# Kernel optimization log

Hardware: AMD Instinct MI355X
Metric: run time of the kernel (lower is better)

Reference implementation:

```python
import jax, jax.numpy as jnp
import numpy as np

BATCH, SEQ, E, H = 8, 2048, 1024, 1024
LEAK = 0.95
SPECTRAL_RADIUS = 1.2
SPARSITY = 0.1


def setup_inputs() -> dict:
    rng = np.random.default_rng(0)
    x = rng.standard_normal((BATCH, SEQ, E)).astype(np.float32)
    # W_in: kaiming_uniform-like init
    bound = np.sqrt(1.0 / E)
    W_in = rng.uniform(-bound, bound, (H, E)).astype(np.float32)
    # W_res: sparse normal, rescaled to spectral radius 1.2
    W_res = rng.standard_normal((H, H)).astype(np.float32)
    mask = (rng.random((H, H)) > SPARSITY).astype(np.float32)
    W_res *= mask
    rad = np.max(np.abs(np.linalg.eigvals(W_res.astype(np.float64))))
    W_res = (W_res * (SPECTRAL_RADIUS / (rad + 1e-8))).astype(np.float32)
    s = 0.02
    inp = {
        "x": jnp.asarray(x),
        "W_in": jnp.asarray(W_in),
        "W_res": jnp.asarray(W_res),
        "norm_g": jnp.ones((E,), jnp.float32),
        "norm_b": jnp.zeros((E,), jnp.float32),
        "delta_w": jnp.asarray(rng.standard_normal((1, E)).astype(np.float32) * s),
        "delta_b": jnp.zeros((1,), jnp.float32),
        "A": jnp.full((H,), -10.0, jnp.float32),
        "B_w": jnp.asarray(rng.standard_normal((H, E)).astype(np.float32) * s),
        "ro_g": jnp.ones((H,), jnp.float32),
        "ro_b": jnp.zeros((H,), jnp.float32),
        "ro_w": jnp.asarray(rng.standard_normal((E, H)).astype(np.float32) * s),
        "ro_bias": jnp.zeros((E,), jnp.float32),
        "gate_w": jnp.asarray(rng.standard_normal((E, E)).astype(np.float32) * s),
        "gate_b": jnp.zeros((E,), jnp.float32),
    }
    return inp


def _layernorm(x, g, b, eps=1e-5):
    m = jnp.mean(x, axis=-1, keepdims=True)
    v = jnp.mean((x - m) ** 2, axis=-1, keepdims=True)
    return (x - m) * jax.lax.rsqrt(v + eps) * g + b


def reference(x, W_in, W_res, norm_g, norm_b, delta_w, delta_b, A, B_w,
              ro_g, ro_b, ro_w, ro_bias, gate_w, gate_b):
    x_norm = _layernorm(x, norm_g, norm_b)                      # [B,S,E]

    # --- TrueReservoir: leaky tanh RNN (scan over seq) ---
    xin = jnp.einsum('bse,he->bsh', x_norm, W_in)               # [B,S,H]
    h0 = jnp.zeros((x.shape[0], W_res.shape[0]), x.dtype)

    def res_step(h, u):
        new = jnp.tanh(u + h @ W_res.T)
        new = LEAK * new + (1.0 - LEAK) * h
        return new, new

    _, res_states = jax.lax.scan(res_step, h0, jnp.swapaxes(xin, 0, 1))
    res_states = jnp.swapaxes(res_states, 0, 1)                 # [B,S,H]

    ro_in = _layernorm(res_states, ro_g, ro_b)
    reservoir_out = jax.nn.gelu(jnp.einsum('bsh,eh->bse', ro_in, ro_w) + ro_bias,
                                approximate=False)              # [B,S,E]

    # --- selective SSM-style scan ---
    Bx = jnp.einsum('bse,he->bsh', x_norm, B_w)                 # [B,S,H]
    delta = jax.nn.softplus(jnp.einsum('bse,oe->bso', x_norm, delta_w) + delta_b)  # [B,S,1]
    A_bar = jnp.exp(A * delta)                                  # [B,S,H]
    B_bar = Bx * (1.0 - A_bar) / (A + 1e-8)                     # [B,S,H]

    def ssm_step(h, ab):
        a, b = ab
        h = a * h + b
        return h, h

    _, ssm_states = jax.lax.scan(
        ssm_step, h0, (jnp.swapaxes(A_bar, 0, 1), jnp.swapaxes(B_bar, 0, 1)))
    ssm_states = jnp.swapaxes(ssm_states, 0, 1)                 # [B,S,H]

    gate = jax.nn.sigmoid(jnp.einsum('bse,fe->bsf', x, gate_w) + gate_b)  # [B,S,E]
    return reservoir_out * gate + ssm_states * (1.0 - gate)
```

## Files before the change

### kernel.cpp

```cpp
#include <hip/hip_runtime.h>
#include <math.h>

#define B_ 8
#define S_ 2048
#define E_ 1024
#define H_ 1024
#define M_ 16384

typedef __attribute__((ext_vector_type(8))) short short8;
typedef __attribute__((ext_vector_type(4))) float floatx4;

__device__ __forceinline__ void block_reduce2(float &a, float &b) {
#pragma unroll
  for (int off = 32; off > 0; off >>= 1) {
    a += __shfl_down(a, off);
    b += __shfl_down(b, off);
  }
  __shared__ float sa[4], sb[4];
  const int w = threadIdx.x >> 6;
  __syncthreads();
  if ((threadIdx.x & 63) == 0) { sa[w] = a; sb[w] = b; }
  __syncthreads();
  a = sa[0] + sa[1] + sa[2] + sa[3];
  b = sb[0] + sb[1] + sb[2] + sb[3];
}

__device__ __forceinline__ unsigned pack_bf16(float lo, float hi) {
  return __builtin_amdgcn_perm(__float_as_uint(hi) + 0x8000u,
                               __float_as_uint(lo) + 0x8000u, 0x07060302u);
}
__device__ __forceinline__ unsigned pack_hi16(unsigned a, unsigned b) {
  return __builtin_amdgcn_perm(b, a, 0x07060302u);
}

__global__ __launch_bounds__(256) void ln_delta_kernel(
    const float* __restrict__ x, const float* __restrict__ g, const float* __restrict__ bt,
    const float* __restrict__ dw, const float* __restrict__ db,
    unsigned short* __restrict__ xnb, float* __restrict__ delta)
{
  const int row = blockIdx.x;
  const int t = threadIdx.x;
  const float4 v = ((const float4*)(x + (size_t)row * E_))[t];
  float s1 = v.x + v.y + v.z + v.w;
  float s2 = v.x*v.x + v.y*v.y + v.z*v.z + v.w*v.w;
  block_reduce2(s1, s2);
  const float mean = s1 * (1.f / E_);
  const float var  = s2 * (1.f / E_) - mean * mean;
  const float rstd = rsqrtf(var + 1e-5f);
  const float4 g4 = ((const float4*)g)[t];
  const float4 b4 = ((const float4*)bt)[t];
  float4 o;
  o.x = (v.x - mean) * rstd * g4.x + b4.x;
  o.y = (v.y - mean) * rstd * g4.y + b4.y;
  o.z = (v.z - mean) * rstd * g4.z + b4.z;
  o.w = (v.w - mean) * rstd * g4.w + b4.w;
  uint2 p;
  p.x = pack_bf16(o.x, o.y); p.y = pack_bf16(o.z, o.w);
  ((uint2*)(xnb + (size_t)row * E_))[t] = p;
  const float4 d4 = ((const float4*)dw)[t];
  float dd = o.x*d4.x + o.y*d4.y + o.z*d4.z + o.w*d4.w;
  float dummy = 0.f;
  block_reduce2(dd, dummy);
  if (t == 0) {
    const float z = dd + db[0];
    delta[row] = (z > 20.f) ? z : log1pf(__expf(z));
  }
}

__global__ __launch_bounds__(256) void rowstats_kernel(
    const float* __restrict__ res, float2* __restrict__ st)
{
  const int row = blockIdx.x;
  const int t = threadIdx.x;
  const float4 v = ((const float4*)(res + (size_t)row * H_))[t];
  float s1 = v.x + v.y + v.z + v.w;
  float s2 = v.x*v.x + v.y*v.y + v.z*v.z + v.w*v.w;
  block_reduce2(s1, s2);
  if (t == 0) {
    const float m = s1 * (1.f / H_);
    const float var = s2 * (1.f / H_) - m * m;
    st[row] = make_float2(m, rsqrtf(var + 1e-5f));
  }
}

__global__ __launch_bounds__(256) void tobf16_kernel(
    const float* __restrict__ s, unsigned short* __restrict__ d)
{
  const int i = blockIdx.x * 256 + threadIdx.x;
  const float4 v = ((const float4*)s)[i];
  uint2 p;
  p.x = pack_bf16(v.x, v.y); p.y = pack_bf16(v.z, v.w);
  ((uint2*)d)[i] = p;
}

__global__ __launch_bounds__(256) void splitw_kernel(
    const float* __restrict__ s, unsigned short* __restrict__ dh, unsigned short* __restrict__ dl)
{
  const int i = blockIdx.x * 256 + threadIdx.x;
  const float4 v = ((const float4*)s)[i];
  const float sv[4] = {v.x, v.y, v.z, v.w};
  unsigned h[4]; float l[4];
#pragma unroll
  for (int e = 0; e < 4; ++e) {
    h[e] = (__float_as_uint(sv[e]) + 0x8000u) & 0xFFFF0000u;
    l[e] = sv[e] - __uint_as_float(h[e]);
  }
  uint2 ph, pl;
  ph.x = pack_hi16(h[0], h[1]); ph.y = pack_hi16(h[2], h[3]);
  pl.x = pack_bf16(l[0], l[1]); pl.y = pack_bf16(l[2], l[3]);
  ((uint2*)dh)[i] = ph;
  ((uint2*)dl)[i] = pl;
}

__global__ __launch_bounds__(256) void gemm_bb(
    const unsigned short* __restrict__ A, const unsigned short* __restrict__ W,
    float* __restrict__ C)
{
  __shared__ __align__(16) unsigned short As[128 * 40];
  __shared__ __align__(16) unsigned short Ws[128 * 40];
  const int tid  = threadIdx.x;
  const int bn   = blockIdx.x & 7;
  const int bm   = blockIdx.x >> 3;
  const int wave = tid >> 6, lane = tid & 63;
  const int wm = (wave >> 1) * 64, wn = (wave & 1) * 64;
  const int fm = lane & 15, quad = lane >> 4;

  floatx4 acc[4][4];
#pragma unroll
  for (int i = 0; i < 4; ++i)
#pragma unroll
    for (int j = 0; j < 4; ++j) acc[i][j] = (floatx4){0.f, 0.f, 0.f, 0.f};

  const unsigned short* Abase = A + (size_t)bm * 128 * 1024;
  const unsigned short* Wbase = W + (size_t)bn * 128 * 1024;

  for (int k0 = 0; k0 < 1024; k0 += 32) {
    uint2 a2[4], w2[4];
#pragma unroll
    for (int i = 0; i < 4; ++i) {
      const int q = tid + 256 * i;
      const int row = q >> 3, ch = q & 7;
      a2[i] = *(const uint2*)(Abase + (size_t)row * 1024 + k0 + ch * 4);
      w2[i] = *(const uint2*)(Wbase + (size_t)row * 1024 + k0 + ch * 4);
    }
#pragma unroll
    for (int i = 0; i < 4; ++i) {
      const int q = tid + 256 * i;
      const int row = q >> 3, ch = q & 7;
      *(uint2*)(&As[row * 40 + ch * 4]) = a2[i];
      *(uint2*)(&Ws[row * 40 + ch * 4]) = w2[i];
    }
    __syncthreads();
    short8 af[4], wf[4];
#pragma unroll
    for (int i = 0; i < 4; ++i) {
      af[i] = *(const short8*)(&As[(wm + i * 16 + fm) * 40 + quad * 8]);
      wf[i] = *(const short8*)(&Ws[(wn + i * 16 + fm) * 40 + quad * 8]);
    }
#pragma unroll
    for (int i = 0; i < 4; ++i)
#pragma unroll
      for (int j = 0; j < 4; ++j)
        acc[i][j] = __builtin_amdgcn_mfma_f32_16x16x32_bf16(af[i], wf[j], acc[i][j], 0, 0, 0);
    __syncthreads();
  }

#pragma unroll
  for (int i = 0; i < 4; ++i) {
    const int grow0 = bm * 128 + wm + i * 16 + quad * 4;
#pragma unroll
    for (int j = 0; j < 4; ++j) {
      const int gcol = bn * 128 + wn + j * 16 + fm;
#pragma unroll
      for (int r = 0; r < 4; ++r)
        C[(size_t)(grow0 + r) * 1024 + gcol] = acc[i][j][r];
    }
  }
}

template<int ACT>
__global__ __launch_bounds__(256) void gemm_bf16_nt(
    const float* __restrict__ A, const float* __restrict__ W,
    const float* __restrict__ bias, float* __restrict__ C)
{
  __shared__ __align__(16) unsigned short As[128 * 40];
  __shared__ __align__(16) unsigned short Ws[128 * 40];
  const int tid  = threadIdx.x;
  const int bn   = blockIdx.x & 7;
  const int bm   = blockIdx.x >> 3;
  const int wave = tid >> 6, lane = tid & 63;
  const int wm = (wave >> 1) * 64, wn = (wave & 1) * 64;
  const int fm = lane & 15, quad = lane >> 4;

  floatx4 acc[4][4];
#pragma unroll
  for (int i = 0; i < 4; ++i)
#pragma unroll
    for (int j = 0; j < 4; ++j) acc[i][j] = (floatx4){0.f, 0.f, 0.f, 0.f};

  const float* Abase = A + (size_t)bm * 128 * 1024;
  const float* Wbase = W + (size_t)bn * 128 * 1024;

  for (int k0 = 0; k0 < 1024; k0 += 32) {
    float4 a4[4], w4[4];
#pragma unroll
    for (int i = 0; i < 4; ++i) {
      const int q = tid + 256 * i;
      const int row = q >> 3, ch = q & 7;
      a4[i] = *(const float4*)(Abase + (size_t)row * 1024 + k0 + ch * 4);
      w4[i] = *(const float4*)(Wbase + (size_t)row * 1024 + k0 + ch * 4);
    }
#pragma unroll
    for (int i = 0; i < 4; ++i) {
      const int q = tid + 256 * i;
      const int row = q >> 3, ch = q & 7;
      uint2 pa, pw;
      pa.x = pack_bf16(a4[i].x, a4[i].y); pa.y = pack_bf16(a4[i].z, a4[i].w);
      pw.x = pack_bf16(w4[i].x, w4[i].y); pw.y = pack_bf16(w4[i].z, w4[i].w);
      *(uint2*)(&As[row * 40 + ch * 4]) = pa;
      *(uint2*)(&Ws[row * 40 + ch * 4]) = pw;
    }
    __syncthreads();
    short8 af[4], wf[4];
#pragma unroll
    for (int i = 0; i < 4; ++i) {
      af[i] = *(const short8*)(&As[(wm + i * 16 + fm) * 40 + quad * 8]);
      wf[i] = *(const short8*)(&Ws[(wn + i * 16 + fm) * 40 + quad * 8]);
    }
#pragma unroll
    for (int i = 0; i < 4; ++i)
#pragma unroll
      for (int j = 0; j < 4; ++j)
        acc[i][j] = __builtin_amdgcn_mfma_f32_16x16x32_bf16(af[i], wf[j], acc[i][j], 0, 0, 0);
    __syncthreads();
  }

#pragma unroll
  for (int i = 0; i < 4; ++i) {
    const int grow0 = bm * 128 + wm + i * 16 + quad * 4;
#pragma unroll
    for (int j = 0; j < 4; ++j) {
      const int gcol = bn * 128 + wn + j * 16 + fm;
      const float bb = (ACT == 1) ? bias[gcol] : 0.f;
#pragma unroll
      for (int r = 0; r < 4; ++r) {
        float v = acc[i][j][r] + bb;
        if (ACT == 1) v = 1.f / (1.f + __expf(-v));
        C[(size_t)(grow0 + r) * 1024 + gcol] = v;
      }
    }
  }
}

__global__ __launch_bounds__(256) void gemm_readout_mfma(
    const float* __restrict__ A,
    const unsigned short* __restrict__ Wh_g,
    const unsigned short* __restrict__ Wl_g,
    const float* __restrict__ bias,
    const float2* __restrict__ lnst,
    const float* __restrict__ lng, const float* __restrict__ lnb,
    const float* __restrict__ Avec,
    const float* __restrict__ cumd,
    const float* __restrict__ chH,
    const float* __restrict__ gate,
    float* __restrict__ C)
{
  __shared__ __align__(16) unsigned short Ah[128 * 40];
  __shared__ __align__(16) unsigned short Al[128 * 40];
  __shared__ __align__(16) unsigned short Wh[128 * 40];
  __shared__ __align__(16) unsigned short Wl[128 * 40];
  const int tid  = threadIdx.x;
  const int bn   = blockIdx.x & 7;
  const int bm   = blockIdx.x >> 3;
  const int wave = tid >> 6, lane = tid & 63;
  const int wm = (wave >> 1) * 64, wn = (wave & 1) * 64;
  const int fm = lane & 15, quad = lane >> 4;

  floatx4 acc[4][4];
#pragma unroll
  for (int i = 0; i < 4; ++i)
#pragma unroll
    for (int j = 0; j < 4; ++j) acc[i][j] = (floatx4){0.f, 0.f, 0.f, 0.f};

  const float* Abase = A + (size_t)bm * 128 * 1024;
  const unsigned short* Whb = Wh_g + (size_t)bn * 128 * 1024;
  const unsigned short* Wlb = Wl_g + (size_t)bn * 128 * 1024;

  float2 st_i[4];
#pragma unroll
  for (int i = 0; i < 4; ++i) {
    const int q = tid + 256 * i;
    st_i[i] = lnst[bm * 128 + (q >> 3)];
  }

  for (int k0 = 0; k0 < 1024; k0 += 32) {
#pragma unroll
    for (int i = 0; i < 4; ++i) {
      const int q = tid + 256 * i;
      const int row = q >> 3, ch = q & 7;
      float4 a4 = *(const float4*)(Abase + (size_t)row * 1024 + k0 + ch * 4);
      const float4 g4 = *(const float4*)(lng + k0 + ch * 4);
      const float4 b4 = *(const float4*)(lnb + k0 + ch * 4);
      const float2 st = st_i[i];
      a4.x = (a4.x - st.x) * st.y * g4.x + b4.x;
      a4.y = (a4.y - st.x) * st.y * g4.y + b4.y;
      a4.z = (a4.z - st.x) * st.y * g4.z + b4.z;
      a4.w = (a4.w - st.x) * st.y * g4.w + b4.w;
      const float av[4] = {a4.x, a4.y, a4.z, a4.w};
      unsigned ah[4]; float alr[4];
#pragma unroll
      for (int e = 0; e < 4; ++e) {
        ah[e] = (__float_as_uint(av[e]) + 0x8000u) & 0xFFFF0000u;
        alr[e] = av[e] - __uint_as_float(ah[e]);
      }
      uint2 pah, pal;
      pah.x = pack_hi16(ah[0], ah[1]); pah.y = pack_hi16(ah[2], ah[3]);
      pal.x = pack_bf16(alr[0], alr[1]); pal.y = pack_bf16(alr[2], alr[3]);
      *(uint2*)(&Ah[row * 40 + ch * 4]) = pah;
      *(uint2*)(&Al[row * 40 + ch * 4]) = pal;
      *(uint2*)(&Wh[row * 40 + ch * 4]) = *(const uint2*)(Whb + (size_t)row * 1024 + k0 + ch * 4);
      *(uint2*)(&Wl[row * 40 + ch * 4]) = *(const uint2*)(Wlb + (size_t)row * 1024 + k0 + ch * 4);
    }
    __syncthreads();
    short8 afh[4], afl[4], wfh[4], wfl[4];
#pragma unroll
    for (int i = 0; i < 4; ++i) {
      const int ao = (wm + i * 16 + fm) * 40 + quad * 8;
      const int wo = (wn + i * 16 + fm) * 40 + quad * 8;
      afh[i] = *(const short8*)(&Ah[ao]);
      afl[i] = *(const short8*)(&Al[ao]);
      wfh[i] = *(const short8*)(&Wh[wo]);
      wfl[i] = *(const short8*)(&Wl[wo]);
    }
#pragma unroll
    for (int i = 0; i < 4; ++i)
#pragma unroll
      for (int j = 0; j < 4; ++j) {
        acc[i][j] = __builtin_amdgcn_mfma_f32_16x16x32_bf16(afh[i], wfh[j], acc[i][j], 0, 0, 0);
        acc[i][j] = __builtin_amdgcn_mfma_f32_16x16x32_bf16(afl[i], wfh[j], acc[i][j], 0, 0, 0);
        acc[i][j] = __builtin_amdgcn_mfma_f32_16x16x32_bf16(afh[i], wfl[j], acc[i][j], 0, 0, 0);
      }
    __syncthreads();
  }

#pragma unroll
  for (int i = 0; i < 4; ++i) {
    const int grow0 = bm * 128 + wm + i * 16 + quad * 4;
    float cd_r[4];
    int hb_r[4];
#pragma unroll
    for (int r = 0; r < 4; ++r) {
      const int gr = grow0 + r;
      const int b = gr >> 11;
      const int c = (gr & 2047) >> 7;
      cd_r[r] = cumd[gr];
      hb_r[r] = (b * 16 + c) << 10;
    }
#pragma unroll
    for (int j = 0; j < 4; ++j) {
      const int gcol = bn * 128 + wn + j * 16 + fm;
      const float Ae = Avec[gcol];
      const float bb = bias[gcol];
#pragma unroll
      for (int r = 0; r < 4; ++r) {
        const int gr = grow0 + r;
        const size_t off = (size_t)gr * 1024 + gcol;
        const float hin = chH[hb_r[r] + gcol];
        const float lcl = C[off];
        const float gt  = gate[off];
        float v = acc[i][j][r] + bb;
        v = 0.5f * v * (1.f + erff(v * 0.70710678118654752f));
        const float p = __expf(Ae * cd_r[r]);
        const float sst = lcl + p * hin;
        C[off] = v * gt + sst * (1.f - gt);
      }
    }
  }
}

__global__ __launch_bounds__(512, 2) void reservoir_scan_kernel(
    float* __restrict__ xin_res,
    const float* __restrict__ Wres,
    unsigned* __restrict__ hbuf,
    unsigned* __restrict__ unused)
{
  const int tid = threadIdx.x;
  const int wg  = blockIdx.x;
  const int go  = wg >> 4;
  const int mem = wg & 15;
  const int g   = tid >> 6;
  const int l   = tid & 63;
  const int c   = l & 7;
  const int rl  = l >> 3;
  const int row = mem * 64 + g * 8 + rl;

  __shared__ __align__(16) float hs[2][1024];

  float4 w4r[32];
  {
    const float* wrow = Wres + (size_t)row * 1024 + c * 128;
#pragma unroll
    for (int i = 0; i < 32; ++i)
      w4r[i] = *(const float4*)(wrow + 4 * ((i + c) & 31));
  }

  float hprev = 0.f;
  const unsigned long long tmask = 0x0000FFFF0000FFFFull;

  for (int s = 0; s < S_; ++s) {
    const float u = xin_res[((size_t)go * S_ + s) * H_ + row];
    asm volatile("" :: "v"(u));

    const unsigned tag = (unsigned)s & 0xFFFFu;
    const unsigned long long tag2 = (unsigned long long)tag | ((unsigned long long)tag << 32);
    const unsigned long long* hp =
        (const unsigned long long*)(hbuf + (size_t)(s & 1) * 8192 + go * 1024) + tid;
    unsigned long long w;
    for (;;) {
      w = __hip_atomic_load(hp, __ATOMIC_RELAXED, __HIP_MEMORY_SCOPE_AGENT);
      if (((w ^ tag2) & tmask) == 0ull) break;
    }

    float2 hf;
    hf.x = __uint_as_float((unsigned)w & 0xFFFF0000u);
    hf.y = __uint_as_float((unsigned)(w >> 32) & 0xFFFF0000u);
    *(float2*)(&hs[s & 1][2 * tid]) = hf;
    __syncthreads();

    const float* hc = &hs[s & 1][c * 128];
    float p0 = 0.f, p1 = 0.f, p2 = 0.f, p3 = 0.f;
#pragma unroll
    for (int i = 0; i < 32; ++i) {
      const float4 h4 = *(const float4*)(hc + 4 * ((i + c) & 31));
      p0 += w4r[i].x * h4.x;
      p1 += w4r[i].y * h4.y;
      p2 += w4r[i].z * h4.z;
      p3 += w4r[i].w * h4.w;
    }
    float ps = (p0 + p1) + (p2 + p3);
    ps += __shfl_xor(ps, 1);
    ps += __shfl_xor(ps, 2);
    ps += __shfl_xor(ps, 4);

    const float z  = u + ps;
    const float e  = __expf(2.f * z);
    const float hn = 1.f - __fdividef(2.f, e + 1.f);
    const float hv = 0.95f * hn + 0.05f * hprev;
    hprev = hv;

    if (c == 0) {
      const unsigned word = ((__float_as_uint(hv) + 0x8000u) & 0xFFFF0000u)
                          | ((unsigned)(s + 1) & 0xFFFFu);
      __hip_atomic_store(hbuf + (size_t)((s + 1) & 1) * 8192 + go * 1024 + row, word,
                         __ATOMIC_RELAXED, __HIP_MEMORY_SCOPE_AGENT);
      xin_res[((size_t)go * S_ + s) * H_ + row] = hv;
    }
  }
}

__global__ __launch_bounds__(128) void cumd_kernel(
    const float* __restrict__ delta, float* __restrict__ cumd)
{
  const int t = threadIdx.x;
  const int b = t >> 4, c = t & 15;
  const int base = b * S_ + c * 128;
  float acc = 0.f;
  for (int i = 0; i < 128; ++i) { acc += delta[base + i]; cumd[base + i] = acc; }
}

__global__ __launch_bounds__(256) void ssm_partial_kernel(
    const float* __restrict__ delta, const float* __restrict__ Avec,
    float* __restrict__ bx, float* __restrict__ P)
{
  const int idx = blockIdx.x * 256 + threadIdx.x;
  const int h = idx & 1023;
  const int c = (idx >> 10) & 15;
  const int b = idx >> 14;
  const float Ah = Avec[h];
  const float inv = 1.f / (Ah + 1e-8f);
  const float* dp = delta + b * S_ + c * 128;
  float* xp = bx + ((size_t)(b * S_ + c * 128)) * H_ + h;
  float p = 1.f, hl = 0.f;
  for (int t = 0; t < 128; ++t) {
    const float a = __expf(Ah * dp[t]);
    const float bb = xp[(size_t)t * H_] * (1.f - a) * inv;
    hl = a * hl + bb;
    p *= a;
    xp[(size_t)t * H_] = hl;
  }
  P[(b * 16 + c) * 1024 + h] = p;
}

__global__ __launch_bounds__(256) void ssm_combine_kernel(
    const float* __restrict__ P, const float* __restrict__ local, float* __restrict__ Hin)
{
  const int idx = blockIdx.x * 256 + threadIdx.x;
  const int h = idx & 1023;
  const int b = idx >> 10;
  float hh = 0.f;
#pragma unroll
  for (int c = 0; c < 16; ++c) {
    const int o = (b * 16 + c) * 1024 + h;
    Hin[o] = hh;
    hh = P[o] * hh + local[((size_t)(b * S_ + c * 128 + 127)) * H_ + h];
  }
}

extern "C" void kernel_launch(void* const* d_in, const int* in_sizes, int n_in,
                              void* d_out, int out_size, void* d_ws, size_t ws_size,
                              hipStream_t stream) {
  (void)in_sizes; (void)n_in; (void)out_size; (void)ws_size;
  const float* x      = (const float*)d_in[0];
  const float* W_in   = (const float*)d_in[1];
  const float* W_res  = (const float*)d_in[2];
  const float* norm_g = (const float*)d_in[3];
  const float* norm_b = (const float*)d_in[4];
  const float* dw     = (const float*)d_in[5];
  const float* db     = (const float*)d_in[6];
  const float* Avec   = (const float*)d_in[7];
  const float* B_w    = (const float*)d_in[8];
  const float* ro_g   = (const float*)d_in[9];
  const float* ro_b   = (const float*)d_in[10];
  const float* ro_w   = (const float*)d_in[11];
  const float* ro_bias= (const float*)d_in[12];
  const float* gate_w = (const float*)d_in[13];
  const float* gate_b = (const float*)d_in[14];
  float* out = (float*)d_out;
  float* ws  = (float*)d_ws;

  float*    buf0   = ws;
  float*    buf1   = ws + 16777216;
  float*    delta  = ws + 33554432;
  float*    cumd   = ws + 33570816;
  unsigned* hbuf   = (unsigned*)(ws + 33587200);
  float2*   stats  = (float2*)(ws + 33603712);
  float*    chP    = ws + 33636480;
  float*    chH    = ws + 33767552;
  unsigned short* xnb = (unsigned short*)buf0;
  unsigned short* wib = (unsigned short*)(ws + 33898624);
  unsigned short* bwb = (unsigned short*)(ws + 34422912);
  unsigned short* roh = (unsigned short*)(ws + 34947200);
  unsigned short* rol = (unsigned short*)(ws + 35471488);

  tobf16_kernel<<<1024, 256, 0, stream>>>(W_in, wib);
  tobf16_kernel<<<1024, 256, 0, stream>>>(B_w, bwb);
  splitw_kernel<<<1024, 256, 0, stream>>>(ro_w, roh, rol);
  ln_delta_kernel<<<M_, 256, 0, stream>>>(x, norm_g, norm_b, dw, db, xnb, delta);
  gemm_bb<<<1024, 256, 0, stream>>>(xnb, wib, buf1);
  gemm_bb<<<1024, 256, 0, stream>>>(xnb, bwb, out);
  gemm_bf16_nt<1><<<1024, 256, 0, stream>>>(x, gate_w, gate_b, buf0);
  cumd_kernel<<<1, 128, 0, stream>>>(delta, cumd);
  ssm_partial_kernel<<<512, 256, 0, stream>>>(delta, Avec, out, chP);
  ssm_combine_kernel<<<32, 256, 0, stream>>>(chP, out, chH);
  hipMemsetAsync(hbuf, 0, 2 * 8192 * sizeof(unsigned), stream);
  reservoir_scan_kernel<<<128, 512, 0, stream>>>(buf1, W_res, hbuf, nullptr);
  rowstats_kernel<<<M_, 256, 0, stream>>>(buf1, stats);
  gemm_readout_mfma<<<1024, 256, 0, stream>>>(buf1, roh, rol, ro_bias, stats, ro_g, ro_b,
                                              Avec, cumd, chH, buf0, out);
}
```

Baseline: 4.135 ms.

## Restructure reservoir matvec so each lane covers 8 rows over a 16-column slice

The reservoir scan's per-step matrix-vector product is re-partitioned. Before, each group of 8 lanes owned one row split into 8 column chunks. Now each lane holds a 16-column slice of all 8 rows its wave owns, so every h float4 read from LDS is reused across 8 rows and each lane does 4 LDS loads per step instead of 32. The h buffer is stored in LDS with an XOR swizzle to avoid bank conflicts, and the partial sums are combined with a transpose-style butterfly shuffle reduction that ends with lanes 0-7 holding the 8 row results. The trade-off is more shuffle steps per step on the serial critical path.

```diff
diff --git a/kernel.cpp b/kernel.cpp
--- a/kernel.cpp
+++ b/kernel.cpp
@@ -390,25 +390,30 @@
   const int mem = wg & 15;
   const int g   = tid >> 6;
   const int l   = tid & 63;
-  const int c   = l & 7;
-  const int rl  = l >> 3;
-  const int row = mem * 64 + g * 8 + rl;
+  const int row8 = mem * 64 + g * 8;
 
   __shared__ __align__(16) float hs[2][1024];
 
-  float4 w4r[32];
+  float4 w4[8][4];
   {
-    const float* wrow = Wres + (size_t)row * 1024 + c * 128;
-#pragma unroll
-    for (int i = 0; i < 32; ++i)
-      w4r[i] = *(const float4*)(wrow + 4 * ((i + c) & 31));
-  }
-
+#pragma unroll
+    for (int r = 0; r < 8; ++r) {
+      const float* wrow = Wres + (size_t)(row8 + r) * 1024 + l * 16;
+#pragma unroll
+      for (int j = 0; j < 4; ++j) w4[r][j] = *(const float4*)(wrow + 4 * j);
+    }
+  }
+
+  const int m0 = l & 1, m1 = (l >> 1) & 1, m2 = (l >> 2) & 1;
+  const int myrow = row8 + (l & 7);
   float hprev = 0.f;
   const unsigned long long tmask = 0x0000FFFF0000FFFFull;
 
+  const int Pw = (tid >> 1) ^ ((tid >> 6) & 7);
+  const int wofs = Pw * 4 + (tid & 1) * 2;
+
   for (int s = 0; s < S_; ++s) {
-    const float u = xin_res[((size_t)go * S_ + s) * H_ + row];
+    const float u = xin_res[((size_t)go * S_ + s) * H_ + myrow];
     asm volatile("" :: "v"(u));
 
     const unsigned tag = (unsigned)s & 0xFFFFu;
@@ -424,23 +429,36 @@
     float2 hf;
     hf.x = __uint_as_float((unsigned)w & 0xFFFF0000u);
     hf.y = __uint_as_float((unsigned)(w >> 32) & 0xFFFF0000u);
-    *(float2*)(&hs[s & 1][2 * tid]) = hf;
-    __syncthreads();
-
-    const float* hc = &hs[s & 1][c * 128];
-    float p0 = 0.f, p1 = 0.f, p2 = 0.f, p3 = 0.f;
-#pragma unroll
-    for (int i = 0; i < 32; ++i) {
-      const float4 h4 = *(const float4*)(hc + 4 * ((i + c) & 31));
-      p0 += w4r[i].x * h4.x;
-      p1 += w4r[i].y * h4.y;
-      p2 += w4r[i].z * h4.z;
-      p3 += w4r[i].w * h4.w;
-    }
-    float ps = (p0 + p1) + (p2 + p3);
-    ps += __shfl_xor(ps, 1);
-    ps += __shfl_xor(ps, 2);
-    ps += __shfl_xor(ps, 4);
+    *(float2*)(&hs[s & 1][wofs]) = hf;
+    __syncthreads();
+
+    const float* hbse = hs[s & 1];
+    float acc0 = 0.f, acc1 = 0.f, acc2 = 0.f, acc3 = 0.f;
+    float acc4 = 0.f, acc5 = 0.f, acc6 = 0.f, acc7 = 0.f;
+#pragma unroll
+    for (int j = 0; j < 4; ++j) {
+      const int P = (4 * l + j) ^ ((l >> 3) & 7);
+      const float4 h4 = *(const float4*)(hbse + P * 4);
+      acc0 += w4[0][j].x * h4.x + w4[0][j].y * h4.y + w4[0][j].z * h4.z + w4[0][j].w * h4.w;
+      acc1 += w4[1][j].x * h4.x + w4[1][j].y * h4.y + w4[1][j].z * h4.z + w4[1][j].w * h4.w;
+      acc2 += w4[2][j].x * h4.x + w4[2][j].y * h4.y + w4[2][j].z * h4.z + w4[2][j].w * h4.w;
+      acc3 += w4[3][j].x * h4.x + w4[3][j].y * h4.y + w4[3][j].z * h4.z + w4[3][j].w * h4.w;
+      acc4 += w4[4][j].x * h4.x + w4[4][j].y * h4.y + w4[4][j].z * h4.z + w4[4][j].w * h4.w;
+      acc5 += w4[5][j].x * h4.x + w4[5][j].y * h4.y + w4[5][j].z * h4.z + w4[5][j].w * h4.w;
+      acc6 += w4[6][j].x * h4.x + w4[6][j].y * h4.y + w4[6][j].z * h4.z + w4[6][j].w * h4.w;
+      acc7 += w4[7][j].x * h4.x + w4[7][j].y * h4.y + w4[7][j].z * h4.z + w4[7][j].w * h4.w;
+    }
+
+    float v0 = (m0 ? acc1 : acc0) + __shfl_xor(m0 ? acc0 : acc1, 1);
+    float v1 = (m0 ? acc3 : acc2) + __shfl_xor(m0 ? acc2 : acc3, 1);
+    float v2 = (m0 ? acc5 : acc4) + __shfl_xor(m0 ? acc4 : acc5, 1);
+    float v3 = (m0 ? acc7 : acc6) + __shfl_xor(m0 ? acc6 : acc7, 1);
+    float u0 = (m1 ? v1 : v0) + __shfl_xor(m1 ? v0 : v1, 2);
+    float u1 = (m1 ? v3 : v2) + __shfl_xor(m1 ? v2 : v3, 2);
+    float ps = (m2 ? u1 : u0) + __shfl_xor(m2 ? u0 : u1, 4);
+    ps += __shfl_xor(ps, 8);
+    ps += __shfl_xor(ps, 16);
+    ps += __shfl_xor(ps, 32);
 
     const float z  = u + ps;
     const float e  = __expf(2.f * z);
@@ -448,12 +466,12 @@
     const float hv = 0.95f * hn + 0.05f * hprev;
     hprev = hv;
 
-    if (c == 0) {
+    if (l < 8) {
       const unsigned word = ((__float_as_uint(hv) + 0x8000u) & 0xFFFF0000u)
                           | ((unsigned)(s + 1) & 0xFFFFu);
-      __hip_atomic_store(hbuf + (size_t)((s + 1) & 1) * 8192 + go * 1024 + row, word,
+      __hip_atomic_store(hbuf + (size_t)((s + 1) & 1) * 8192 + go * 1024 + myrow, word,
                          __ATOMIC_RELAXED, __HIP_MEMORY_SCOPE_AGENT);
-      xin_res[((size_t)go * S_ + s) * H_ + row] = hv;
+      xin_res[((size_t)go * S_ + s) * H_ + myrow] = hv;
     }
   }
 }
```

Measured after the change: 3.989 ms. 1.04x faster.
